# Kernel tuning notes

Hardware: AMD Instinct MI355X
Metric: run time of the kernel (lower is better)

Reference implementation:

```python
import jax, jax.numpy as jnp
import numpy as np

B = 2048          # batch
D = 256           # agent input dim
S = 32            # num_splines
CANVAS = 128      # canvas_size
NUM_T = 50        # samples along each Bezier curve (hard-coded in module)
BRUSH = 1         # brush_size (hard-coded)
SCALE = 1e-4      # Normal scale hard-coded in forward (log_std is unused)
W_STAMP = -0.07   # per-stamp weight (hard-coded)
BG = 0.3          # background_shade


def setup_inputs() -> dict:
    key = jax.random.key(0)
    k1, k2 = jax.random.split(key, 2)
    x = jax.random.normal(k1, (B, D), dtype=jnp.float32)
    W_agent = jax.random.normal(k2, (D, S * 6), dtype=jnp.float32) * 0.05
    b_agent = jnp.zeros((S * 6,), dtype=jnp.float32)
    return {"x": x, "W_agent": W_agent, "b_agent": b_agent}


def _paint_multiple_splines(sample):
    # sample: [B, S*6] in (0,1)
    bsz = sample.shape[0]
    params = sample.reshape(bsz, -1, 6) * CANVAS          # [B, S, 6]
    P0 = params[..., 0:2][:, :, None, :]                   # [B, S, 1, 2]
    P1 = params[..., 2:4][:, :, None, :]
    P2 = params[..., 4:6][:, :, None, :]
    t = jnp.linspace(0.0, 1.0, NUM_T, dtype=params.dtype).reshape(1, 1, NUM_T, 1)
    # quadratic Bezier: [B, S, T, 2]
    spline_points = (1 - t) ** 2 * P0 + 2 * (1 - t) * t * P1 + t ** 2 * P2
    coords = jnp.round(spline_points).astype(jnp.int32)
    r = jnp.arange(-BRUSH, BRUSH + 1)
    dx, dy = jnp.meshgrid(r, r, indexing="ij")
    dx, dy = dx.ravel(), dy.ravel()                        # [9]
    x_idx = jnp.clip(coords[..., 0][..., None] + dx, 0, CANVAS - 1)  # [B,S,T,9]
    y_idx = jnp.clip(coords[..., 1][..., None] + dy, 0, CANVAS - 1)
    flat_idx = (x_idx * CANVAS + y_idx).reshape(bsz, -1)   # [B, S*T*9]
    weights = jnp.full(flat_idx.shape, W_STAMP, dtype=jnp.float32)
    canvas_flat = jnp.zeros((bsz, CANVAS * CANVAS), dtype=jnp.float32)
    canvas_flat = canvas_flat.at[jnp.arange(bsz)[:, None], flat_idx].add(weights)
    canvas = canvas_flat.reshape(bsz, CANVAS, CANVAS)
    return jnp.clip(canvas + BG, 0.0, 1.0)


def reference(x, W_agent, b_agent):
    mu = x @ W_agent + b_agent                             # [B, S*6]
    scale = jnp.float32(SCALE)
    log2pi = jnp.log(jnp.float32(2.0) * jnp.pi)
    dim = mu.shape[-1]
    # eval-time path: raw_sample = mu
    raw = mu
    log_prob = jnp.sum(
        -0.5 * ((raw - mu) / scale) ** 2 - jnp.log(scale) - 0.5 * log2pi,
        axis=-1,
    )                                                      # [B]
    entropy = jnp.full(
        (mu.shape[0],), dim * (0.5 + 0.5 * log2pi + jnp.log(scale)),
        dtype=jnp.float32,
    )                                                      # [B]
    sample = jax.nn.sigmoid(raw)                           # [B, S*6]
    sketch = _paint_multiple_splines(sample)               # [B, CANVAS, CANVAS]
    return sketch, log_prob, entropy, sample
```

## Files before the change

kernel.cpp:

```cpp
#include <hip/hip_runtime.h>
#include <math.h>

#define NB      2048
#define DIM     256
#define SC6     192
#define CV      128
#define NT      50
#define NBPB    2

#define LPV  (1591.9491530441301f)
#define ENV  (-1495.9491530441301f)

#define SKETCH_N   ((size_t)NB * CV * CV)
#define LP_OFF     (SKETCH_N)
#define ENT_OFF    (LP_OFF + NB)
#define SAMPLE_OFF (ENT_OFF + NB)

typedef float vfloat4 __attribute__((ext_vector_type(4)));

__global__ __launch_bounds__(512) void fused_kernel(
    const float* __restrict__ x, const float* __restrict__ W,
    const float* __restrict__ bias, float* __restrict__ out)
{
    __shared__ unsigned int cnt[CV * CV / 4];
    __shared__ double sp[NBPB][6][32];
    __shared__ double cfa[NT], cfb[NT], cfc[NT];

    const int b0  = blockIdx.x * NBPB;
    const int tid = threadIdx.x;

    if (tid < SC6) {
        const int j = tid;
        const float* xb0 = x + (size_t)b0 * DIM;
        const float* xb1 = xb0 + DIM;
        double a0 = 0.0, a1 = 0.0;
        #pragma unroll 8
        for (int d = 0; d < DIM; ++d) {
            double wd = (double)W[d * SC6 + j];
            a0 = fma((double)xb0[d], wd, a0);
            a1 = fma((double)xb1[d], wd, a1);
        }
        double bj = (double)bias[j];
        double s0 = 1.0 / (1.0 + exp(-(a0 + bj)));
        double s1 = 1.0 / (1.0 + exp(-(a1 + bj)));
        out[SAMPLE_OFF + (size_t)b0 * SC6 + j]       = (float)s0;
        out[SAMPLE_OFF + (size_t)(b0 + 1) * SC6 + j] = (float)s1;
        sp[0][j % 6][j / 6] = s0 * 128.0;
        sp[1][j % 6][j / 6] = s1 * 128.0;
    } else {
        const int t2 = tid - SC6;
        uint4* c4 = (uint4*)cnt;
        uint4 z = make_uint4(0u, 0u, 0u, 0u);
        for (int w = t2; w < 1024; w += 320) c4[w] = z;
        if (t2 < NT) {
            double t = (t2 == NT - 1) ? 1.0 : (double)t2 * (1.0 / 49.0);
            double u = 1.0 - t;
            cfa[t2] = u * u;
            cfb[t2] = (2.0 * u) * t;
            cfc[t2] = t * t;
        }
        if (t2 == 60) out[LP_OFF  + b0]     = LPV;
        if (t2 == 61) out[ENT_OFF + b0]     = ENV;
        if (t2 == 62) out[LP_OFF  + b0 + 1] = LPV;
        if (t2 == 63) out[ENT_OFF + b0 + 1] = ENV;
    }
    __syncthreads();

    #pragma unroll
    for (int bb = 0; bb < NBPB; ++bb) {
        for (int i = tid; i < 32 * NT; i += 512) {
            int s = i & 31;
            int k = i >> 5;
            double a  = cfa[k];
            double bq = cfb[k];
            double c  = cfc[k];
            double px = a * sp[bb][0][s] + bq * sp[bb][2][s] + c * sp[bb][4][s];
            double py = a * sp[bb][1][s] + bq * sp[bb][3][s] + c * sp[bb][5][s];
            int cx = (int)rint(px);
            int cy = (int)rint(py);

            int y0 = min(max(cy - 1, 0), CV - 1);
            int y1 = min(max(cy,     0), CV - 1);
            int y2 = min(max(cy + 1, 0), CV - 1);
            int cb = y0 >> 2;
            unsigned incA = 1u << ((y0 & 3) << 3);
            unsigned incB = 0u;
            unsigned i1 = 1u << ((y1 & 3) << 3);
            unsigned i2 = 1u << ((y2 & 3) << 3);
            if ((y1 >> 2) == cb) incA += i1; else incB += i1;
            if ((y2 >> 2) == cb) incA += i2; else incB += i2;

            int x0 = min(max(cx - 1, 0), CV - 1);
            int x1 = min(max(cx,     0), CV - 1);
            int x2 = min(max(cx + 1, 0), CV - 1);
            int rows[3] = {x0, x1, x2};
            #pragma unroll
            for (int r = 0; r < 3; ++r) {
                int xi = rows[r];
                int base = xi << 5;
                atomicAdd(&cnt[base + ((cb + xi) & 31)], incA);
                if (incB) atomicAdd(&cnt[base + ((cb + 1 + xi) & 31)], incB);
            }
        }
        __syncthreads();

        vfloat4* ob = (vfloat4*)(out + (size_t)(b0 + bb) * CV * CV);
        for (int w = tid; w < CV * CV / 4; w += 512) {
            int xi  = w >> 5;
            int idx = (xi << 5) + (((w & 31) + xi) & 31);
            unsigned v = cnt[idx];
            cnt[idx] = 0u;
            vfloat4 r;
            r.x = fminf(fmaxf(0.3f - 0.07f * (float)( v        & 255u), 0.0f), 1.0f);
            r.y = fminf(fmaxf(0.3f - 0.07f * (float)((v >>  8) & 255u), 0.0f), 1.0f);
            r.z = fminf(fmaxf(0.3f - 0.07f * (float)((v >> 16) & 255u), 0.0f), 1.0f);
            r.w = fminf(fmaxf(0.3f - 0.07f * (float)( v >> 24        ), 0.0f), 1.0f);
            __builtin_nontemporal_store(r, &ob[w]);
        }
        if (bb + 1 < NBPB) __syncthreads();
    }
}

extern "C" void kernel_launch(void* const* d_in, const int* in_sizes, int n_in,
                              void* d_out, int out_size, void* d_ws, size_t ws_size,
                              hipStream_t stream) {
    const float* x    = (const float*)d_in[0];
    const float* W    = (const float*)d_in[1];
    const float* bias = (const float*)d_in[2];
    float* out = (float*)d_out;

    fused_kernel<<<NB / NBPB, 512, 0, stream>>>(x, W, bias, out);
}
```

Measured before the change: 163.8 us.

## Split fused kernel into batched GEMM kernel and per-sample paint kernel

```diff
diff --git a/kernel.cpp b/kernel.cpp
--- a/kernel.cpp
+++ b/kernel.cpp
@@ -6,7 +6,7 @@
 #define SC6     192
 #define CV      128
 #define NT      50
-#define NBPB    2
+#define BPB     8
 
 #define LPV  (1591.9491530441301f)
 #define ENV  (-1495.9491530441301f)
@@ -18,40 +18,66 @@
 
 typedef float vfloat4 __attribute__((ext_vector_type(4)));
 
-__global__ __launch_bounds__(512) void fused_kernel(
+__global__ __launch_bounds__(192) void gemm_kernel(
     const float* __restrict__ x, const float* __restrict__ W,
-    const float* __restrict__ bias, float* __restrict__ out)
+    const float* __restrict__ bias, float* __restrict__ out,
+    double* __restrict__ params)
+{
+    __shared__ float xs[BPB][DIM];
+    const int b0  = blockIdx.x * BPB;
+    const int tid = threadIdx.x;
+
+    for (int i = tid; i < BPB * DIM; i += 192) {
+        int bl = i >> 8;
+        int d  = i & 255;
+        xs[bl][d] = x[(size_t)(b0 + bl) * DIM + d];
+    }
+    __syncthreads();
+
+    const int j = tid;
+    double acc[BPB] = {0, 0, 0, 0, 0, 0, 0, 0};
+
+    #pragma unroll 4
+    for (int d = 0; d < DIM; ++d) {
+        double wd = (double)W[d * SC6 + j];
+        #pragma unroll
+        for (int bl = 0; bl < BPB; ++bl)
+            acc[bl] = fma((double)xs[bl][d], wd, acc[bl]);
+    }
+
+    const double bj = (double)bias[j];
+    #pragma unroll
+    for (int bl = 0; bl < BPB; ++bl) {
+        double s = 1.0 / (1.0 + exp(-(acc[bl] + bj)));
+        out[SAMPLE_OFF + (size_t)(b0 + bl) * SC6 + j] = (float)s;
+        params[(size_t)(b0 + bl) * SC6 + j] = s * 128.0;
+    }
+
+    if (tid < BPB)           out[LP_OFF  + b0 + tid]       = LPV;
+    else if (tid < 2 * BPB)  out[ENT_OFF + b0 + tid - BPB] = ENV;
+}
+
+__global__ __launch_bounds__(256) void paint_kernel(
+    const double* __restrict__ params, float* __restrict__ out)
 {
     __shared__ unsigned int cnt[CV * CV / 4];
-    __shared__ double sp[NBPB][6][32];
+    __shared__ double sp[6][32];
     __shared__ double cfa[NT], cfb[NT], cfc[NT];
 
-    const int b0  = blockIdx.x * NBPB;
+    const int b   = blockIdx.x;
     const int tid = threadIdx.x;
 
-    if (tid < SC6) {
-        const int j = tid;
-        const float* xb0 = x + (size_t)b0 * DIM;
-        const float* xb1 = xb0 + DIM;
-        double a0 = 0.0, a1 = 0.0;
-        #pragma unroll 8
-        for (int d = 0; d < DIM; ++d) {
-            double wd = (double)W[d * SC6 + j];
-            a0 = fma((double)xb0[d], wd, a0);
-            a1 = fma((double)xb1[d], wd, a1);
-        }
-        double bj = (double)bias[j];
-        double s0 = 1.0 / (1.0 + exp(-(a0 + bj)));
-        double s1 = 1.0 / (1.0 + exp(-(a1 + bj)));
-        out[SAMPLE_OFF + (size_t)b0 * SC6 + j]       = (float)s0;
-        out[SAMPLE_OFF + (size_t)(b0 + 1) * SC6 + j] = (float)s1;
-        sp[0][j % 6][j / 6] = s0 * 128.0;
-        sp[1][j % 6][j / 6] = s1 * 128.0;
-    } else {
-        const int t2 = tid - SC6;
+    {
         uint4* c4 = (uint4*)cnt;
         uint4 z = make_uint4(0u, 0u, 0u, 0u);
-        for (int w = t2; w < 1024; w += 320) c4[w] = z;
+        #pragma unroll
+        for (int w = 0; w < 4; ++w) c4[tid + 256 * w] = z;
+    }
+    if (tid < SC6) {
+        double v = params[(size_t)b * SC6 + tid];
+        sp[tid % 6][tid / 6] = v;
+    } else {
+        int t2 = tid - SC6;
         if (t2 < NT) {
             double t = (t2 == NT - 1) ? 1.0 : (double)t2 * (1.0 / 49.0);
             double u = 1.0 - t;
@@ -59,65 +85,56 @@
             cfb[t2] = (2.0 * u) * t;
             cfc[t2] = t * t;
         }
-        if (t2 == 60) out[LP_OFF  + b0]     = LPV;
-        if (t2 == 61) out[ENT_OFF + b0]     = ENV;
-        if (t2 == 62) out[LP_OFF  + b0 + 1] = LPV;
-        if (t2 == 63) out[ENT_OFF + b0 + 1] = ENV;
     }
     __syncthreads();
 
-    #pragma unroll
-    for (int bb = 0; bb < NBPB; ++bb) {
-        for (int i = tid; i < 32 * NT; i += 512) {
-            int s = i & 31;
-            int k = i >> 5;
-            double a  = cfa[k];
-            double bq = cfb[k];
-            double c  = cfc[k];
-            double px = a * sp[bb][0][s] + bq * sp[bb][2][s] + c * sp[bb][4][s];
-            double py = a * sp[bb][1][s] + bq * sp[bb][3][s] + c * sp[bb][5][s];
-            int cx = (int)rint(px);
-            int cy = (int)rint(py);
+    for (int i = tid; i < 32 * NT; i += 256) {
+        int s = i & 31;
+        int k = i >> 5;
+        double a  = cfa[k];
+        double bq = cfb[k];
+        double c  = cfc[k];
+        double px = a * sp[0][s] + bq * sp[2][s] + c * sp[4][s];
+        double py = a * sp[1][s] + bq * sp[3][s] + c * sp[5][s];
+        int cx = (int)rint(px);
+        int cy = (int)rint(py);
 
-            int y0 = min(max(cy - 1, 0), CV - 1);
-            int y1 = min(max(cy,     0), CV - 1);
-            int y2 = min(max(cy + 1, 0), CV - 1);
-            int cb = y0 >> 2;
-            unsigned incA = 1u << ((y0 & 3) << 3);
-            unsigned incB = 0u;
-            unsigned i1 = 1u << ((y1 & 3) << 3);
-            unsigned i2 = 1u << ((y2 & 3) << 3);
-            if ((y1 >> 2) == cb) incA += i1; else incB += i1;
-            if ((y2 >> 2) == cb) incA += i2; else incB += i2;
+        int y0 = min(max(cy - 1, 0), CV - 1);
+        int y1 = min(max(cy,     0), CV - 1);
+        int y2 = min(max(cy + 1, 0), CV - 1);
+        int cb = y0 >> 2;
+        unsigned incA = 1u << ((y0 & 3) << 3);
+        unsigned incB = 0u;
+        unsigned i1 = 1u << ((y1 & 3) << 3);
+        unsigned i2 = 1u << ((y2 & 3) << 3);
+        if ((y1 >> 2) == cb) incA += i1; else incB += i1;
+        if ((y2 >> 2) == cb) incA += i2; else incB += i2;
 
-            int x0 = min(max(cx - 1, 0), CV - 1);
-            int x1 = min(max(cx,     0), CV - 1);
-            int x2 = min(max(cx + 1, 0), CV - 1);
-            int rows[3] = {x0, x1, x2};
-            #pragma unroll
-            for (int r = 0; r < 3; ++r) {
-                int xi = rows[r];
-                int base = xi << 5;
-                atomicAdd(&cnt[base + ((cb + xi) & 31)], incA);
-                if (incB) atomicAdd(&cnt[base + ((cb + 1 + xi) & 31)], incB);
-            }
+        int x0 = min(max(cx - 1, 0), CV - 1);
+        int x1 = min(max(cx,     0), CV - 1);
+        int x2 = min(max(cx + 1, 0), CV - 1);
+        int rows[3] = {x0, x1, x2};
+        #pragma unroll
+        for (int r = 0; r < 3; ++r) {
+            int xi = rows[r];
+            int base = xi << 5;
+            atomicAdd(&cnt[base + ((cb + xi) & 31)], incA);
+            if (incB) atomicAdd(&cnt[base + ((cb + 1 + xi) & 31)], incB);
         }
-        __syncthreads();
+    }
+    __syncthreads();
 
-        vfloat4* ob = (vfloat4*)(out + (size_t)(b0 + bb) * CV * CV);
-        for (int w = tid; w < CV * CV / 4; w += 512) {
-            int xi  = w >> 5;
-            int idx = (xi << 5) + (((w & 31) + xi) & 31);
-            unsigned v = cnt[idx];
-            cnt[idx] = 0u;
-            vfloat4 r;
-            r.x = fminf(fmaxf(0.3f - 0.07f * (float)( v        & 255u), 0.0f), 1.0f);
-            r.y = fminf(fmaxf(0.3f - 0.07f * (float)((v >>  8) & 255u), 0.0f), 1.0f);
-            r.z = fminf(fmaxf(0.3f - 0.07f * (float)((v >> 16) & 255u), 0.0f), 1.0f);
-            r.w = fminf(fmaxf(0.3f - 0.07f * (float)( v >> 24        ), 0.0f), 1.0f);
-            __builtin_nontemporal_store(r, &ob[w]);
-        }
-        if (bb + 1 < NBPB) __syncthreads();
+    vfloat4* ob = (vfloat4*)(out + (size_t)b * CV * CV);
+    for (int w = tid; w < CV * CV / 4; w += 256) {
+        int xi  = w >> 5;
+        int idx = (xi << 5) + (((w & 31) + xi) & 31);
+        unsigned v = cnt[idx];
+        vfloat4 r;
+        r.x = fminf(fmaxf(0.3f - 0.07f * (float)( v        & 255u), 0.0f), 1.0f);
+        r.y = fminf(fmaxf(0.3f - 0.07f * (float)((v >>  8) & 255u), 0.0f), 1.0f);
+        r.z = fminf(fmaxf(0.3f - 0.07f * (float)((v >> 16) & 255u), 0.0f), 1.0f);
+        r.w = fminf(fmaxf(0.3f - 0.07f * (float)( v >> 24        ), 0.0f), 1.0f);
+        __builtin_nontemporal_store(r, &ob[w]);
     }
 }
 
@@ -128,6 +145,8 @@
     const float* W    = (const float*)d_in[1];
     const float* bias = (const float*)d_in[2];
     float* out = (float*)d_out;
+    double* params = (double*)d_ws;
 
-    fused_kernel<<<NB / NBPB, 512, 0, stream>>>(x, W, bias, out);
+    gemm_kernel<<<NB / BPB, 192, 0, stream>>>(x, W, bias, out, params);
+    paint_kernel<<<NB, 256, 0, stream>>>(params, out);
 }
```

New measurement: 185.8 us. 13.4% more time.
